# Kernel optimization log

Measured on AMD Instinct MI355X. Metric: run time of the kernel, lower is better.

## Reference

```python
import jax, jax.numpy as jnp
import numpy as np
from math import sqrt

NUM_HEADS = 16
DIM_MODEL = 1024


def setup_inputs() -> dict:
    key = jax.random.key(0)
    ks = jax.random.split(key, 12)
    B, S, D, M = 4, 1024, DIM_MODEL, 64
    bound = 1.0 / sqrt(D)
    def lin_w(k):
        return jax.random.uniform(k, (D, D), jnp.float32, -bound, bound)
    def lin_b(k):
        return jax.random.uniform(k, (D,), jnp.float32, -bound, bound)
    return {
        "query": jax.random.normal(ks[0], (B, S, D), jnp.float32),
        "key": jax.random.normal(ks[1], (B, S, D), jnp.float32),
        "value": jax.random.normal(ks[2], (B, S, D), jnp.float32),
        "mask": jax.random.randint(ks[3], (1, B, S, M), 0, 2).astype(jnp.float32),
        "Wq": lin_w(ks[4]), "bq": lin_b(ks[5]),
        "Wk": lin_w(ks[6]), "bk": lin_b(ks[7]),
        "Wv": lin_w(ks[8]), "bv": lin_b(ks[9]),
        "Wo": lin_w(ks[10]),
    }


def reference(query, key, value, mask, Wq, bq, Wk, bk, Wv, bv, Wo):
    B, S, D = query.shape
    H = NUM_HEADS
    d = D // H
    # projections + head split, permute(2,0,1,3) -> [H,B,S,d]
    q = (query @ Wq.T + bq).reshape(B, S, H, d).transpose(2, 0, 1, 3)
    k = (key @ Wk.T + bk).reshape(B, S, H, d).transpose(2, 0, 1, 3)
    v = (value @ Wv.T + bv).reshape(B, S, H, d).transpose(2, 0, 1, 3)
    attn = jnp.einsum("hbqd,hbkd->hbqk", q, k) / sqrt(d)  # [H,B,S,S]
    # custom mask: mask.repeat(H,1,1,1) then mask @ mask^T / sqrt(m).
    # Identical per-head, so compute once on [B,S,m] and broadcast over H.
    m2d = mask[0]  # [B,S,m]
    mm = jnp.einsum("bqm,bkm->bqk", m2d, m2d) / sqrt(m2d.shape[-1])
    attn = jnp.where(mm[None] == 0, jnp.float32(-1e9), attn)
    w = jax.nn.softmax(attn, axis=-1)  # dropout is identity in eval mode
    x = jnp.einsum("hbqk,hbkd->hbqd", w, v)  # [H,B,S,d]
    # torch: permute(1,2,0,3) -> [B,S,H,d]; transpose(1,2) -> [B,H,S,d];
    # contiguous().view(B,-1,H*d) -- row-major reshape (mixes head/seq layout, replicated faithfully)
    x = jnp.transpose(x, (1, 0, 2, 3))  # [B,H,S,d]
    x = x.reshape(B, -1, H * d)
    return x @ Wo.T
```

## Files before the change

kernel.cpp:

```cpp
#include <hip/hip_runtime.h>

typedef unsigned int u32;
typedef unsigned short u16;
typedef unsigned long long u64;
typedef __attribute__((ext_vector_type(8))) short s16x8;
typedef __attribute__((ext_vector_type(8))) __bf16 bf16x8;
typedef __attribute__((ext_vector_type(4))) float f32x4;
typedef __attribute__((ext_vector_type(16))) float f32x16;
typedef __attribute__((ext_vector_type(4))) u32 u32x4;

#define WSMB (1ull << 20)
#define QSC 0.18033688011112042f

static __device__ __forceinline__ u16 f2bf(float f) {
  u32 u = __builtin_bit_cast(u32, f);
  return (u16)((u + 0x7fffu + ((u >> 16) & 1u)) >> 16);
}

static __device__ __forceinline__ u32 pkbf(float lo, float hi) {
  u32 r;
  asm("v_cvt_pk_bf16_f32 %0, %1, %2" : "=v"(r) : "v"(lo), "v"(hi));
  return r;
}

static __device__ __forceinline__ float ex2(float x) {
  float r;
  asm("v_exp_f32 %0, %1" : "=v"(r) : "v"(x));
  return r;
}

static __device__ __forceinline__ f32x4 mfma16x16(s16x8 a, s16x8 b, f32x4 c) {
  return __builtin_amdgcn_mfma_f32_16x16x32_bf16(
      __builtin_bit_cast(bf16x8, a), __builtin_bit_cast(bf16x8, b), c, 0, 0, 0);
}

static __device__ __forceinline__ f32x16 mfma32x32(s16x8 a, s16x8 b, f32x16 c) {
  return __builtin_amdgcn_mfma_f32_32x32x16_bf16(
      __builtin_bit_cast(bf16x8, a), __builtin_bit_cast(bf16x8, b), c, 0, 0, 0);
}

#define GLOAD_LDS16(g, l)                                                      \
  __builtin_amdgcn_global_load_lds(                                            \
      (const __attribute__((address_space(1))) u32*)(const void*)(g),          \
      (__attribute__((address_space(3))) u32*)(void*)(l), 16, 0, 0)

__global__ __launch_bounds__(256) void k_prep(
    const float* __restrict__ xq, const float* __restrict__ xk,
    const float* __restrict__ xv, const float* __restrict__ wq,
    const float* __restrict__ wk, const float* __restrict__ wv,
    const float* __restrict__ wo, const float* __restrict__ mask,
    u16* __restrict__ oxq, u16* __restrict__ oxk, u16* __restrict__ oxv,
    u16* __restrict__ owq, u16* __restrict__ owk, u16* __restrict__ owv,
    u16* __restrict__ owo, u64* __restrict__ bits) {
  const int y = blockIdx.y;
  if (y >= 3 && blockIdx.x >= 1024) return;
  if (y == 7) {
    int w = threadIdx.x >> 6, l = threadIdx.x & 63;
    int r = blockIdx.x * 4 + w;
    float v = mask[(size_t)r * 64 + l];
    u64 bl = __ballot(v != 0.0f);
    if (l == 0) bits[r] = bl;
    return;
  }
  const float* s;
  u16* d;
  switch (y) {
    case 0: s = xq; d = oxq; break;
    case 1: s = xk; d = oxk; break;
    case 2: s = xv; d = oxv; break;
    case 3: s = wq; d = owq; break;
    case 4: s = wk; d = owk; break;
    case 5: s = wv; d = owv; break;
    default: s = wo; d = owo; break;
  }
  int i = (blockIdx.x * 256 + threadIdx.x) * 4;
  float4 v = *(const float4*)(s + i);
  u64 p = (u64)f2bf(v.x) | ((u64)f2bf(v.y) << 16) | ((u64)f2bf(v.z) << 32) |
          ((u64)f2bf(v.w) << 48);
  *(u64*)(d + i) = p;
}

__global__ __launch_bounds__(256) void k_mm(const u64* __restrict__ bits,
                                            u64* __restrict__ MB) {
  int wv = threadIdx.x >> 6, l = threadIdx.x & 63;
  int qg = blockIdx.x * 4 + wv;
  u64 bq = bits[qg];
  const u64* bb = bits + (qg & ~1023);
  u64* out = MB + (size_t)qg * 16;
  for (int kt = 0; kt < 16; kt++) {
    u64 bk = bb[kt * 64 + l];
    u64 m = __ballot((bq & bk) != 0ull);
    if (l == 0) out[kt] = m;
  }
}

static __device__ __forceinline__ void gemm_core(const u16* __restrict__ A,
                                                 const u16* __restrict__ Bw,
                                                 f32x4 (&acc)[4][4]) {
  __shared__ __attribute__((aligned(16))) u16 As[2][4096];
  __shared__ __attribute__((aligned(16))) u16 Bs[2][4096];
  const int t = threadIdx.x;
  const int l = t & 63, w = t >> 6, lr = l & 15, lk = l >> 4;
  const int amr = (w & 1) * 64, bnr = (w >> 1) * 64;
  const int c0 = t, c1 = t + 256;
  const int r0 = c0 >> 2, r1 = c1 >> 2;
  const int sw0 = ((c0 & 3) * 8) ^ ((r0 & 6) << 2);
  const int sw1 = ((c1 & 3) * 8) ^ ((r1 & 6) << 2);
  const u16* Ag0 = A + (size_t)r0 * 1024 + sw0;
  const u16* Ag1 = A + (size_t)r1 * 1024 + sw1;
  const u16* Bg0 = Bw + (size_t)r0 * 1024 + sw0;
  const u16* Bg1 = Bw + (size_t)r1 * 1024 + sw1;
  const int aswz = (lk * 16) ^ ((lr & 6) << 3);

  GLOAD_LDS16(Ag0, &As[0][c0 * 8]);
  GLOAD_LDS16(Ag1, &As[0][c1 * 8]);
  GLOAD_LDS16(Bg0, &Bs[0][c0 * 8]);
  GLOAD_LDS16(Bg1, &Bs[0][c1 * 8]);

  int cur = 0;
  for (int kt = 0; kt < 1024; kt += 32) {
    __syncthreads();
    if (kt < 992) {
      const int nxt = cur ^ 1;
      GLOAD_LDS16(Ag0 + kt + 32, &As[nxt][c0 * 8]);
      GLOAD_LDS16(Ag1 + kt + 32, &As[nxt][c1 * 8]);
      GLOAD_LDS16(Bg0 + kt + 32, &Bs[nxt][c0 * 8]);
      GLOAD_LDS16(Bg1 + kt + 32, &Bs[nxt][c1 * 8]);
    }
    const char* Ac = (const char*)As[cur];
    const char* Bc = (const char*)Bs[cur];
    s16x8 af[4], bf[4];
#pragma unroll
    for (int i = 0; i < 4; i++)
      af[i] = *(const s16x8*)(Ac + (amr + i * 16 + lr) * 64 + aswz);
#pragma unroll
    for (int j = 0; j < 4; j++)
      bf[j] = *(const s16x8*)(Bc + (bnr + j * 16 + lr) * 64 + aswz);
    __builtin_amdgcn_s_setprio(1);
#pragma unroll
    for (int i = 0; i < 4; i++)
#pragma unroll
      for (int j = 0; j < 4; j++)
        acc[i][j] = mfma16x16(af[i], bf[j], acc[i][j]);
    __builtin_amdgcn_s_setprio(0);
    cur ^= 1;
  }
}

__global__ __launch_bounds__(256) void k_qkv(
    const u16* __restrict__ Xq, const u16* __restrict__ Xk,
    const u16* __restrict__ Xv, const u16* __restrict__ Wqb,
    const u16* __restrict__ Wkb, const u16* __restrict__ Wvb,
    const float* __restrict__ bq, const float* __restrict__ bk,
    const float* __restrict__ bv, u16* __restrict__ Qo, u16* __restrict__ Ko,
    u16* __restrict__ V4) {
  const int bid0 = blockIdx.x;
  const int bid = (bid0 & 7) * 96 + (bid0 >> 3);
  const int proj = bid >> 8;
  const int rem = bid & 255;
  const int st = rem >> 3, dt = rem & 7;
  const u16* Xp = proj == 0 ? Xq : (proj == 1 ? Xk : Xv);
  const u16* Wp = proj == 0 ? Wqb : (proj == 1 ? Wkb : Wvb);
  const float* bias = proj == 0 ? bq : (proj == 1 ? bk : bv);
  const int t = threadIdx.x;
  const int l = t & 63, w = t >> 6, lr = l & 15, lk = l >> 4;
  const int amr = (w & 1) * 64, bnr = (w >> 1) * 64;
  f32x4 acc[4][4] = {};
  if (proj < 2) {
    const float sc = proj == 0 ? QSC : 1.0f;
    gemm_core(Wp + (size_t)dt * 131072, Xp + (size_t)st * 131072, acc);
    u16* O = proj ? Ko : Qo;
#pragma unroll
    for (int i = 0; i < 4; i++) {
      const int d0 = dt * 128 + amr + i * 16 + lk * 4;
      const int h = d0 >> 6, dd0 = d0 & 63;
      const float4 b4 = *(const float4*)(bias + d0);
#pragma unroll
      for (int j = 0; j < 4; j++) {
        const int s = st * 128 + bnr + j * 16 + lr;
        const int b_ = s >> 10, si = s & 1023;
        u32 e0 = pkbf((acc[i][j][0] + b4.x) * sc, (acc[i][j][1] + b4.y) * sc);
        u32 e1 = pkbf((acc[i][j][2] + b4.z) * sc, (acc[i][j][3] + b4.w) * sc);
        *(u64*)(O + ((size_t)((b_ * 16 + h) * 1024 + si)) * 64 + dd0) =
            (u64)e0 | ((u64)e1 << 32);
      }
    }
  } else {
    gemm_core(Xp + (size_t)st * 131072, Wp + (size_t)dt * 131072, acc);
#pragma unroll
    for (int i = 0; i < 4; i++) {
      const int s0 = st * 128 + amr + i * 16 + lk * 4;
      const int b_ = s0 >> 10, si = s0 & 1023;
      const int sblk = si >> 3, soff = si & 7;
#pragma unroll
      for (int j = 0; j < 4; j++) {
        const int d = dt * 128 + bnr + j * 16 + lr;
        const int h = d >> 6, dd = d & 63;
        const float bb = bias[d];
        u32 e0 = pkbf(acc[i][j][0] + bb, acc[i][j][1] + bb);
        u32 e1 = pkbf(acc[i][j][2] + bb, acc[i][j][3] + bb);
        *(u64*)(V4 + (size_t)(b_ * 16 + h) * 65536 +
                (size_t)(sblk * 64 + dd) * 8 + soff) =
            (u64)e0 | ((u64)e1 << 32);
      }
    }
  }
}

__global__ __launch_bounds__(256) void k_oproj(const u16* __restrict__ Xb,
                                               const u16* __restrict__ Wob,
                                               float* __restrict__ Out) {
  const int bid0 = blockIdx.x;
  const int bid = (bid0 & 7) * 32 + (bid0 >> 3);
  const int mb = bid >> 3, nb = bid & 7;
  f32x4 acc[4][4] = {};
  gemm_core(Xb + (size_t)mb * 131072, Wob + (size_t)nb * 131072, acc);
  const int t = threadIdx.x;
  const int l = t & 63, w = t >> 6, lr = l & 15, lk = l >> 4;
  const int amr = (w & 1) * 64, bnr = (w >> 1) * 64;
#pragma unroll
  for (int i = 0; i < 4; i++)
#pragma unroll
    for (int j = 0; j < 4; j++)
#pragma unroll
      for (int r = 0; r < 4; r++) {
        const int m = mb * 128 + amr + i * 16 + lk * 4 + r;
        const int n = nb * 128 + bnr + j * 16 + lr;
        Out[(size_t)m * 1024 + n] = acc[i][j][r];
      }
}

__global__ __launch_bounds__(128, 2) void k_attn(const u16* __restrict__ Qb,
                                                 const u16* __restrict__ Kb,
                                                 const u16* __restrict__ V4,
                                                 const u64* __restrict__ MB,
                                                 u16* __restrict__ xbuf) {
  __shared__ __attribute__((aligned(16))) u16 Ks[2][4096];
  __shared__ __attribute__((aligned(16))) u16 Vs[2][4096];
  const int t = threadIdx.x, l = t & 63, w = t >> 6;
  const int q5 = l & 31, hi = l >> 5;
  const int bid = (blockIdx.x & 7) * 128 + (blockIdx.x >> 3);
  const int qt = bid & 15, hb = bid >> 4;
  const int h = hb >> 2, b = hb & 3;
  const int s0 = qt * 64;
  const u16* Qhb = Qb + (size_t)(b * 16 + h) * 65536;
  const u16* Khb = Kb + (size_t)(b * 16 + h) * 65536;
  const u16* Vhb = V4 + (size_t)(b * 16 + h) * 65536;
  const int q = s0 + w * 32 + q5;
  const u64* MBq = MB + ((size_t)b * 1024 + q) * 16;

  s16x8 qf[4];
#pragma unroll
  for (int ds = 0; ds < 4; ds++)
    qf[ds] = *(const s16x8*)(Qhb + (size_t)q * 64 + ds * 16 + hi * 8);

  f32x16 xa0 = {}, xa1 = {};
  float ls = 0.f, m_ = -__builtin_inff();

  const u16 *Kg[4], *Vg[4];
  int cdst[4];
#pragma unroll
  for (int i = 0; i < 4; i++) {
    const int c = t + i * 128;
    const int r_ = c >> 3, col = (c & 7) * 16;
    const int s_ = col ^ ((r_ & 7) << 4);
    Kg[i] = Khb + (size_t)r_ * 64 + (s_ >> 1);
    Vg[i] = Vhb + (size_t)(s_ >> 4) * 512 + r_ * 8;
    cdst[i] = c * 8;
  }

  const int rbase = q5 * 128 + ((hi * 16) ^ ((q5 & 7) << 4));

#pragma unroll
  for (int i = 0; i < 4; i++) {
    GLOAD_LDS16(Kg[i], &Ks[0][cdst[i]]);
    GLOAD_LDS16(Vg[i], &Vs[0][cdst[i]]);
  }
  u64 mw = MBq[0];

  int cur = 0;
  for (int kt = 0; kt < 16; kt++) {
    __syncthreads();
    if (kt < 15) {
      const int nxt = cur ^ 1;
#pragma unroll
      for (int i = 0; i < 4; i++) {
        GLOAD_LDS16(Kg[i] + (kt + 1) * 4096, &Ks[nxt][cdst[i]]);
        GLOAD_LDS16(Vg[i] + (kt + 1) * 4096, &Vs[nxt][cdst[i]]);
      }
    }
    const u64 nw = MBq[(kt + 1) & 15];
    const char* Kc = (const char*)Ks[cur];
    const char* Vc = (const char*)Vs[cur];

    f32x16 z0 = {}, z1 = {};
#pragma unroll
    for (int ds = 0; ds < 4; ds++) {
      s16x8 k0 = *(const s16x8*)(Kc + (rbase ^ (ds * 32)));
      s16x8 k1 = *(const s16x8*)(Kc + 4096 + (rbase ^ (ds * 32)));
      __builtin_amdgcn_s_setprio(1);
      z0 = mfma32x32(k0, qf[ds], z0);
      z1 = mfma32x32(k1, qf[ds], z1);
      __builtin_amdgcn_s_setprio(0);
    }

    float tmx[16];
#pragma unroll
    for (int r = 0; r < 16; r++) tmx[r] = fmaxf(z0[r], z1[r]);
#pragma unroll
    for (int st_ = 8; st_ >= 1; st_ >>= 1)
#pragma unroll
      for (int r = 0; r < 8; r++)
        if (r < st_) tmx[r] = fmaxf(tmx[r], tmx[r + st_]);
    float tm = tmx[0];
    tm = fmaxf(tm, __shfl_xor(tm, 32));
    if (tm > m_) {
      const float scl = ex2(m_ - tm);
      m_ = tm;
      ls *= scl;
      xa0 *= scl;
      xa1 *= scl;
    }

    float e0[16], e1[16];
#pragma unroll
    for (int r = 0; r < 16; r++) e0[r] = ex2(z0[r] - m_);
#pragma unroll
    for (int r = 0; r < 16; r++) e1[r] = ex2(z1[r] - m_);
    if (!__all(mw == ~0ull)) {
      const u32 mh0 = (u32)(mw >> (hi * 4));
      const u32 mh1 = (u32)(mw >> (hi * 4 + 32));
#pragma unroll
      for (int r = 0; r < 16; r++) {
        const int bp = 8 * (r >> 2) + (r & 3);
        e0[r] = ((mh0 >> bp) & 1u) ? e0[r] : 0.f;
        e1[r] = ((mh1 >> bp) & 1u) ? e1[r] : 0.f;
      }
    }
    float ts = 0.f;
#pragma unroll
    for (int r = 0; r < 16; r++) ts += e0[r] + e1[r];
    ls += ts;

    u32 P0[2][4], P1[2][4];
#pragma unroll
    for (int qi = 0; qi < 4; qi++) {
      P0[0][qi] = pkbf(e0[4 * qi], e0[4 * qi + 1]);
      P1[0][qi] = pkbf(e0[4 * qi + 2], e0[4 * qi + 3]);
      P0[1][qi] = pkbf(e1[4 * qi], e1[4 * qi + 1]);
      P1[1][qi] = pkbf(e1[4 * qi + 2], e1[4 * qi + 3]);
    }

#pragma unroll
    for (int ks = 0; ks < 4; ks++) {
      const int kb = ks >> 1, qi0 = (ks & 1) * 2, qi1 = qi0 + 1;
      u32 w0 = P0[kb][qi0], w2 = P0[kb][qi1];
      u32 w1 = P1[kb][qi0], w3 = P1[kb][qi1];
      asm("v_permlane32_swap_b32 %0, %1" : "+v"(w0), "+v"(w2));
      asm("v_permlane32_swap_b32 %0, %1" : "+v"(w1), "+v"(w3));
      u32x4 fv;
      fv[0] = w0; fv[1] = w1; fv[2] = w2; fv[3] = w3;
      const s16x8 pb = __builtin_bit_cast(s16x8, fv);
      s16x8 v0 = *(const s16x8*)(Vc + (rbase ^ (ks * 32)));
      s16x8 v1 = *(const s16x8*)(Vc + 4096 + (rbase ^ (ks * 32)));
      __builtin_amdgcn_s_setprio(1);
      xa0 = mfma32x32(v0, pb, xa0);
      xa1 = mfma32x32(v1, pb, xa1);
      __builtin_amdgcn_s_setprio(0);
    }
    mw = nw;
    cur ^= 1;
  }

  ls += __shfl_xor(ls, 32);
  const float inv = 1.0f / ls;
  const size_t rowb = (size_t)b * 1048576 + (size_t)(h * 64 + (q >> 4)) * 1024 +
                      (size_t)(q & 15) * 64;
#pragma unroll
  for (int qi = 0; qi < 4; qi++) {
    u32 a0 = pkbf(xa0[4 * qi] * inv, xa0[4 * qi + 1] * inv);
    u32 a1 = pkbf(xa0[4 * qi + 2] * inv, xa0[4 * qi + 3] * inv);
    *(u64*)(xbuf + rowb + 8 * qi + 4 * hi) = (u64)a0 | ((u64)a1 << 32);
    u32 b0 = pkbf(xa1[4 * qi] * inv, xa1[4 * qi + 1] * inv);
    u32 b1 = pkbf(xa1[4 * qi + 2] * inv, xa1[4 * qi + 3] * inv);
    *(u64*)(xbuf + rowb + 32 + 8 * qi + 4 * hi) = (u64)b0 | ((u64)b1 << 32);
  }
}

extern "C" void kernel_launch(void* const* d_in, const int* in_sizes, int n_in,
                              void* d_out, int out_size, void* d_ws,
                              size_t ws_size, hipStream_t stream) {
  const float* query = (const float*)d_in[0];
  const float* key_ = (const float*)d_in[1];
  const float* value = (const float*)d_in[2];
  const float* mask = (const float*)d_in[3];
  const float* bq = (const float*)d_in[5];
  const float* bk = (const float*)d_in[7];
  const float* bv = (const float*)d_in[9];
  const float* Wq = (const float*)d_in[4];
  const float* Wk = (const float*)d_in[6];
  const float* Wv = (const float*)d_in[8];
  const float* Wo = (const float*)d_in[10];

  char* ws = (char*)d_ws;
  u16* Xq = (u16*)(ws + 0 * WSMB);
  u16* Xk = (u16*)(ws + 8 * WSMB);
  u16* Xv = (u16*)(ws + 16 * WSMB);
  u16* Wqb = (u16*)(ws + 24 * WSMB);
  u16* Wkb = (u16*)(ws + 26 * WSMB);
  u16* Wvb = (u16*)(ws + 28 * WSMB);
  u16* Wob = (u16*)(ws + 30 * WSMB);
  u16* Qb = (u16*)(ws + 32 * WSMB);
  u16* Kb = (u16*)(ws + 40 * WSMB);
  u16* V4 = (u16*)(ws + 48 * WSMB);
  u64* bits = (u64*)(ws + 56 * WSMB);
  u64* MBm = (u64*)(ws + 8 * WSMB);
  u16* xbuf = Xq;

  k_prep<<<dim3(4096, 8), 256, 0, stream>>>(query, key_, value, Wq, Wk, Wv, Wo,
                                            mask, Xq, Xk, Xv, Wqb, Wkb, Wvb,
                                            Wob, bits);
  k_qkv<<<768, 256, 0, stream>>>(Xq, Xk, Xv, Wqb, Wkb, Wvb, bq, bk, bv, Qb, Kb,
                                 V4);
  k_mm<<<1024, 256, 0, stream>>>(bits, MBm);
  k_attn<<<1024, 128, 0, stream>>>(Qb, Kb, V4, MBm, xbuf);
  k_oproj<<<256, 256, 0, stream>>>(xbuf, Wob, (float*)d_out);
}
```

Baseline: 120.7 us.

## Load K/V fragments directly from global memory instead of LDS double buffering

The attention kernel drops the shared-memory double-buffered K/V tiles, along with their async global-to-LDS copies and per-iteration barriers. Each wave now loads its MFMA operand fragments for K and V straight from global memory into registers at the start of every key tile. This removes the LDS traffic and __syncthreads, but both waves in a block now fetch the same K/V data redundantly. There is also no explicit prefetch, so global latency sits on the critical path unless the compiler hoists the loads. Register pressure rises because 16 extra 128-bit fragments are held live.

Measured after the change: 129.4 us. 1.07x slower.

```diff
diff --git a/kernel.cpp b/kernel.cpp
--- a/kernel.cpp
+++ b/kernel.cpp
@@ -235,8 +235,6 @@
                                                  const u16* __restrict__ V4,
                                                  const u64* __restrict__ MB,
                                                  u16* __restrict__ xbuf) {
-  __shared__ __attribute__((aligned(16))) u16 Ks[2][4096];
-  __shared__ __attribute__((aligned(16))) u16 Vs[2][4096];
   const int t = threadIdx.x, l = t & 63, w = t >> 6;
   const int q5 = l & 31, hi = l >> 5;
   const int bid = (blockIdx.x & 7) * 128 + (blockIdx.x >> 3);
@@ -257,52 +255,37 @@
   f32x16 xa0 = {}, xa1 = {};
   float ls = 0.f, m_ = -__builtin_inff();
 
-  const u16 *Kg[4], *Vg[4];
-  int cdst[4];
-#pragma unroll
-  for (int i = 0; i < 4; i++) {
-    const int c = t + i * 128;
-    const int r_ = c >> 3, col = (c & 7) * 16;
-    const int s_ = col ^ ((r_ & 7) << 4);
-    Kg[i] = Khb + (size_t)r_ * 64 + (s_ >> 1);
-    Vg[i] = Vhb + (size_t)(s_ >> 4) * 512 + r_ * 8;
-    cdst[i] = c * 8;
-  }
-
-  const int rbase = q5 * 128 + ((hi * 16) ^ ((q5 & 7) << 4));
-
-#pragma unroll
-  for (int i = 0; i < 4; i++) {
-    GLOAD_LDS16(Kg[i], &Ks[0][cdst[i]]);
-    GLOAD_LDS16(Vg[i], &Vs[0][cdst[i]]);
-  }
+  const u16* Kr0 = Khb + (size_t)q5 * 64 + hi * 8;
+  const u16* Kr1 = Khb + (size_t)(32 + q5) * 64 + hi * 8;
+  const u16* Vr0 = Vhb + (size_t)q5 * 8;
+  const u16* Vr1 = Vhb + (size_t)(32 + q5) * 8;
+
   u64 mw = MBq[0];
-
-  int cur = 0;
   for (int kt = 0; kt < 16; kt++) {
-    __syncthreads();
-    if (kt < 15) {
-      const int nxt = cur ^ 1;
-#pragma unroll
-      for (int i = 0; i < 4; i++) {
-        GLOAD_LDS16(Kg[i] + (kt + 1) * 4096, &Ks[nxt][cdst[i]]);
-        GLOAD_LDS16(Vg[i] + (kt + 1) * 4096, &Vs[nxt][cdst[i]]);
-      }
+    const int ko = kt * 4096;
+    const int vb = kt * 8 + hi;
+    s16x8 k0[4], k1[4];
+#pragma unroll
+    for (int ds = 0; ds < 4; ds++) {
+      k0[ds] = *(const s16x8*)(Kr0 + ko + ds * 16);
+      k1[ds] = *(const s16x8*)(Kr1 + ko + ds * 16);
+    }
+    s16x8 v0[4], v1[4];
+#pragma unroll
+    for (int ks = 0; ks < 4; ks++) {
+      v0[ks] = *(const s16x8*)(Vr0 + (size_t)(vb + 2 * ks) * 512);
+      v1[ks] = *(const s16x8*)(Vr1 + (size_t)(vb + 2 * ks) * 512);
     }
     const u64 nw = MBq[(kt + 1) & 15];
-    const char* Kc = (const char*)Ks[cur];
-    const char* Vc = (const char*)Vs[cur];
 
     f32x16 z0 = {}, z1 = {};
+    __builtin_amdgcn_s_setprio(1);
 #pragma unroll
     for (int ds = 0; ds < 4; ds++) {
-      s16x8 k0 = *(const s16x8*)(Kc + (rbase ^ (ds * 32)));
-      s16x8 k1 = *(const s16x8*)(Kc + 4096 + (rbase ^ (ds * 32)));
-      __builtin_amdgcn_s_setprio(1);
-      z0 = mfma32x32(k0, qf[ds], z0);
-      z1 = mfma32x32(k1, qf[ds], z1);
-      __builtin_amdgcn_s_setprio(0);
-    }
+      z0 = mfma32x32(k0[ds], qf[ds], z0);
+      z1 = mfma32x32(k1[ds], qf[ds], z1);
+    }
+    __builtin_amdgcn_s_setprio(0);
 
     float tmx[16];
 #pragma unroll
@@ -353,23 +336,20 @@
 
 #pragma unroll
     for (int ks = 0; ks < 4; ks++) {
-      const int kb = ks >> 1, qi0 = (ks & 1) * 2, qi1 = qi0 + 1;
-      u32 w0 = P0[kb][qi0], w2 = P0[kb][qi1];
-      u32 w1 = P1[kb][qi0], w3 = P1[kb][qi1];
+      const int kb_ = ks >> 1, qi0 = (ks & 1) * 2, qi1 = qi0 + 1;
+      u32 w0 = P0[kb_][qi0], w2 = P0[kb_][qi1];
+      u32 w1 = P1[kb_][qi0], w3 = P1[kb_][qi1];
       asm("v_permlane32_swap_b32 %0, %1" : "+v"(w0), "+v"(w2));
       asm("v_permlane32_swap_b32 %0, %1" : "+v"(w1), "+v"(w3));
       u32x4 fv;
       fv[0] = w0; fv[1] = w1; fv[2] = w2; fv[3] = w3;
       const s16x8 pb = __builtin_bit_cast(s16x8, fv);
-      s16x8 v0 = *(const s16x8*)(Vc + (rbase ^ (ks * 32)));
-      s16x8 v1 = *(const s16x8*)(Vc + 4096 + (rbase ^ (ks * 32)));
       __builtin_amdgcn_s_setprio(1);
-      xa0 = mfma32x32(v0, pb, xa0);
-      xa1 = mfma32x32(v1, pb, xa1);
+      xa0 = mfma32x32(v0[ks], pb, xa0);
+      xa1 = mfma32x32(v1[ks], pb, xa1);
       __builtin_amdgcn_s_setprio(0);
     }
     mw = nw;
-    cur ^= 1;
   }
 
   ls += __shfl_xor(ls, 32);
```
